# Performance work log

Hardware: AMD Instinct MI355X
Metric: run time of the kernel (lower is better)

The kernel has to match this reference:

```python
import jax, jax.numpy as jnp
import numpy as np

E = 8        # num_workers / experts
D = 1024     # decoder_embed_dim
F = 4096     # decoder_ffn_embed_dim
S, B = 2048, 2
LN_EPS = 1e-5


def setup_inputs() -> dict:
    key = jax.random.key(0)
    ks = jax.random.split(key, 8)
    scale_in = 1.0 / np.sqrt(D)
    scale_ff = 1.0 / np.sqrt(F)
    return {
        "input_features": jax.random.normal(ks[0], (S, B, D), dtype=jnp.float32),
        "centroids": jax.random.normal(ks[1], (E, D), dtype=jnp.float32) * scale_in,  # Linear(D, E, bias=False) weight
        "ln_g": jnp.ones((E, D), dtype=jnp.float32),
        "ln_b": jnp.zeros((E, D), dtype=jnp.float32),
        "W1": jax.random.normal(ks[2], (E, D, F), dtype=jnp.float32) * scale_in,
        "b1": jax.random.normal(ks[3], (E, F), dtype=jnp.float32) * 0.01,
        "W2": jax.random.normal(ks[4], (E, F, D), dtype=jnp.float32) * scale_ff,  # original zero-inits; random for non-trivial reference
        "b2": jax.random.normal(ks[5], (E, D), dtype=jnp.float32) * 0.01,
    }


def _moe_forward(input_features, centroids, ln_g, ln_b, W1, b1, W2, b2):
    s, b, d = input_features.shape
    # [S,B,D] -> transpose(0,1) -> [B,S,D] -> flatten tokens
    x = jnp.swapaxes(input_features, 0, 1).reshape(-1, d)  # [T, D]
    # fp32 gating, top-1 (greedy) assignment; BASE layer does NOT scale by gate prob
    logits = x.astype(jnp.float32) @ centroids.astype(jnp.float32).T  # [T, E]
    assign = jnp.argmax(logits, axis=-1)                              # [T]
    onehot = jax.nn.one_hot(assign, E, dtype=x.dtype)                 # [T, E]
    # dispatch: zero out tokens not assigned to expert e  -> [E, T, D]
    disp = jnp.einsum("te,td->etd", onehot, x)
    # expert-local MoESublayer: xs + ff2(relu(ff1(LN(xs))))
    mu = disp.mean(-1, keepdims=True)
    var = disp.var(-1, keepdims=True)
    xn = (disp - mu) * jax.lax.rsqrt(var + LN_EPS)
    xn = xn * ln_g[:, None, :] + ln_b[:, None, :]
    h = jax.nn.relu(jnp.einsum("etd,edf->etf", xn, W1) + b1[:, None, :])
    y = jnp.einsum("etf,efd->etd", h, W2) + b2[:, None, :]
    y = disp + y  # residual
    # combine: pick assigned expert's output per token (sort+all2all+inverse-sort == identity permutation here)
    out = jnp.einsum("te,etd->td", onehot, y)  # [T, D]
    return jnp.swapaxes(out.reshape(b, s, d), 0, 1)  # back to [S, B, D]


def reference(input_features, centroids, ln_g, ln_b, W1, b1, W2, b2):
    return _moe_forward(input_features, centroids, ln_g, ln_b, W1, b1, W2, b2)
```

## Files before the change

### kernel.cpp

```cpp
#include <hip/hip_runtime.h>
#include <hip/hip_bf16.h>

#define E_ 8
#define D_ 1024
#define F_ 4096
#define S_ 2048
#define B_ 2
#define T_ 4096
#define CAP 1024
#define LN_EPS 1e-5f
#define MAXTAB 40

typedef __attribute__((ext_vector_type(8))) short short8;
typedef __attribute__((ext_vector_type(4))) float f32x4;

__device__ __forceinline__ unsigned short f2bf(float f) {
  __hip_bfloat16 h = __float2bfloat16(f);
  return *reinterpret_cast<unsigned short*>(&h);
}

__global__ __launch_bounds__(256) void gate_ln_kernel(
    const float* __restrict__ x, const float* __restrict__ cent,
    const float* __restrict__ g_, const float* __restrict__ bb_,
    const float* __restrict__ b2_,
    int* __restrict__ counts, int* __restrict__ perm,
    unsigned short* __restrict__ Xb, float* __restrict__ outp) {
  int token = blockIdx.x * 4 + (threadIdx.x >> 6);
  int lane = threadIdx.x & 63;
  int s = token & (S_ - 1), b = token >> 11;
  const float* xr = x + ((size_t)s * B_ + b) * D_;
  float* orow = outp + ((size_t)s * B_ + b) * D_;

  float v[16];
  float acc[E_];
#pragma unroll
  for (int e = 0; e < E_; ++e) acc[e] = 0.f;
  float sum = 0.f, sq = 0.f;
#pragma unroll
  for (int c = 0; c < 4; ++c) {
    f32x4 xv = *(const f32x4*)(xr + c * 256 + lane * 4);
    v[c * 4 + 0] = xv.x; v[c * 4 + 1] = xv.y; v[c * 4 + 2] = xv.z; v[c * 4 + 3] = xv.w;
    sum += xv.x + xv.y + xv.z + xv.w;
    sq += xv.x * xv.x + xv.y * xv.y + xv.z * xv.z + xv.w * xv.w;
#pragma unroll
    for (int e = 0; e < E_; ++e) {
      f32x4 cv = *(const f32x4*)(cent + e * D_ + c * 256 + lane * 4);
      acc[e] += xv.x * cv.x + xv.y * cv.y + xv.z * cv.z + xv.w * cv.w;
    }
  }
#pragma unroll
  for (int off = 32; off > 0; off >>= 1) {
    sum += __shfl_down(sum, off);
    sq += __shfl_down(sq, off);
#pragma unroll
    for (int e = 0; e < E_; ++e) acc[e] += __shfl_down(acc[e], off);
  }
  int best = 0, slot = 0;
  if (lane == 0) {
    float bv = acc[0];
#pragma unroll
    for (int e = 1; e < E_; ++e) if (acc[e] > bv) { bv = acc[e]; best = e; }
    slot = atomicAdd(&counts[best], 1);
    perm[best * CAP + slot] = token;
  }
  best = __shfl(best, 0); slot = __shfl(slot, 0);
  sum = __shfl(sum, 0); sq = __shfl(sq, 0);
  float mu = sum * (1.f / D_);
  float var = sq * (1.f / D_) - mu * mu;
  float rstd = rsqrtf(var + LN_EPS);
  int e = best;
  unsigned short* dst = Xb + (size_t)(e * CAP + slot) * D_;
#pragma unroll
  for (int c = 0; c < 4; ++c) {
    int d = c * 256 + lane * 4;
    f32x4 gv = *(const f32x4*)(g_ + e * D_ + d);
    f32x4 bv = *(const f32x4*)(bb_ + e * D_ + d);
    f32x4 b2v = *(const f32x4*)(b2_ + e * D_ + d);
    ushort4 o;
    o.x = f2bf((v[c * 4 + 0] - mu) * rstd * gv.x + bv.x);
    o.y = f2bf((v[c * 4 + 1] - mu) * rstd * gv.y + bv.y);
    o.z = f2bf((v[c * 4 + 2] - mu) * rstd * gv.z + bv.z);
    o.w = f2bf((v[c * 4 + 3] - mu) * rstd * gv.w + bv.w);
    *(ushort4*)(dst + d) = o;
    f32x4 oi;
    oi.x = v[c * 4 + 0] + b2v.x; oi.y = v[c * 4 + 1] + b2v.y;
    oi.z = v[c * 4 + 2] + b2v.z; oi.w = v[c * 4 + 3] + b2v.w;
    *(f32x4*)(orow + d) = oi;
  }
}

__global__ void prefix_kernel(const int* __restrict__ counts, int* __restrict__ offs,
                              int* __restrict__ tab) {
  if (threadIdx.x == 0) {
    int s = 0, t = 0;
    for (int e = 0; e < E_; ++e) {
      offs[e] = s;
      int nb = (counts[e] + 127) >> 7;
      for (int m = 0; m < nb; ++m) tab[t++] = (e << 16) | m;
      s += counts[e];
    }
    offs[E_] = s;
    for (; t < MAXTAB; ++t) tab[t] = -1;
  }
}

template <int K, int N, int MODE, int KSPLIT>
__global__ __launch_bounds__(256, 3) void moe_gemm_kernel(
    const unsigned short* __restrict__ A,
    const float* __restrict__ W,
    const float* __restrict__ bias,
    const int* __restrict__ counts,
    const int* __restrict__ offs,
    const int* __restrict__ tab,
    const int* __restrict__ perm,
    void* __restrict__ outp) {
  const int tentry = tab[blockIdx.y];
  if (tentry < 0) return;
  const int e = tentry >> 16;
  const int m0 = (tentry & 0xffff) << 7;
  const int cnt = counts[e];
  if (m0 >= cnt) return;
  const int aoff = (MODE == 0) ? e * CAP : offs[e];
  const int hoff = offs[e];
  const int n0 = blockIdx.x * 128;
  const int kstart = blockIdx.z * (K / KSPLIT);
  constexpr int NSTEP = (K / KSPLIT) / 32;
  static_assert(NSTEP >= 4 && (NSTEP % 2) == 0, "NSTEP must be even >= 4");

  const int tid = threadIdx.x;
  const int lane = tid & 63;
  const int wave = tid >> 6;

  __shared__ __align__(16) unsigned short lA[2][4096];
  __shared__ __align__(16) unsigned short lB[2][4096];

  const int ra = tid & 127;
  const int qa = tid >> 7;
  const int arow = aoff + min(m0 + ra, cnt - 1);
  const unsigned short* asrc = A + (size_t)arow * K + kstart + qa * 8;

  const float* wsrc = W + (size_t)e * K * N + (size_t)(kstart + wave * 8) * N + n0 + lane;

  f32x4 acc[4][4] = {};
  const int wr = (wave >> 1) * 64;
  const int wc = (wave & 1) * 64;
  const int fr = lane & 15;
  const int fq = lane >> 4;

  short8 pA00, pA01, pA10, pA11;
  float pBa0[8], pBb0[8], pBa1[8], pBb1[8];

  pA00 = *(const short8*)(asrc);
  pA01 = *(const short8*)(asrc + 16);
#pragma unroll
  for (int j = 0; j < 8; ++j) {
    pBa0[j] = wsrc[(size_t)j * N];
    pBb0[j] = wsrc[(size_t)j * N + 64];
  }
  pA10 = *(const short8*)(asrc + 32);
  pA11 = *(const short8*)(asrc + 48);
  {
    const float* wp_ = wsrc + (size_t)32 * N;
#pragma unroll
    for (int j = 0; j < 8; ++j) {
      pBa1[j] = wp_[(size_t)j * N];
      pBb1[j] = wp_[(size_t)j * N + 64];
    }
  }
  *(short8*)&lA[0][qa * 1024 + ra * 8] = pA00;
  *(short8*)&lA[0][(qa + 2) * 1024 + ra * 8] = pA01;
  {
    short8 c0_, c1_;
#pragma unroll
    for (int j = 0; j < 8; ++j) {
      c0_[j] = (short)f2bf(pBa0[j]);
      c1_[j] = (short)f2bf(pBb0[j]);
    }
    *(short8*)&lB[0][wave * 1024 + lane * 8] = c0_;
    *(short8*)&lB[0][wave * 1024 + (lane + 64) * 8] = c1_;
  }
  asm volatile("s_waitcnt lgkmcnt(0)" ::: "memory");
  __builtin_amdgcn_s_barrier();
  asm volatile("" ::: "memory");

#define STEP_BODY(TV, CUR, NXT)                                                     \
  {                                                                                 \
    const int tv_ = (TV);                                                           \
    if (tv_ + 2 < NSTEP) {            \
      const unsigned short* ap_ = asrc + (tv_ + 2) * 32;                            \
      pA##CUR##0 = *(const short8*)ap_;                                             \
      pA##CUR##1 = *(const short8*)(ap_ + 16);                                      \
      const float* wp_ = wsrc + (size_t)(tv_ + 2) * 32 * N;                         \
      _Pragma("unroll") for (int j = 0; j < 8; ++j) {                               \
        pBa##CUR[j] = wp_[(size_t)j * N];                                           \
        pBb##CUR[j] = wp_[(size_t)j * N + 64];                                      \
      }                                                                             \
    }                                                                               \
    if (tv_ + 1 < NSTEP) {        \
      *(short8*)&lA[NXT][qa * 1024 + ra * 8] = pA##NXT##0;                          \
      *(short8*)&lA[NXT][(qa + 2) * 1024 + ra * 8] = pA##NXT##1;                    \
      short8 c0_, c1_;                                                              \
      _Pragma("unroll") for (int j = 0; j < 8; ++j) {                               \
        c0_[j] = (short)f2bf(pBa##NXT[j]);                                          \
        c1_[j] = (short)f2bf(pBb##NXT[j]);                                          \
      }                                                                             \
      *(short8*)&lB[NXT][wave * 1024 + lane * 8] = c0_;                             \
      *(short8*)&lB[NXT][wave * 1024 + (lane + 64) * 8] = c1_;                      \
    }                                                                               \
    short8 af_[4], bf_[4];                                                          \
    _Pragma("unroll") for (int m = 0; m < 4; ++m)                                   \
        af_[m] = *(const short8*)&lA[CUR][fq * 1024 + (wr + m * 16 + fr) * 8];      \
    _Pragma("unroll") for (int n = 0; n < 4; ++n)                                   \
        bf_[n] = *(const short8*)&lB[CUR][fq * 1024 + (wc + n * 16 + fr) * 8];      \
    __builtin_amdgcn_s_setprio(1);                                                  \
    _Pragma("unroll") for (int m = 0; m < 4; ++m)                                   \
        _Pragma("unroll") for (int n = 0; n < 4; ++n)                               \
            acc[m][n] =                                                             \
                __builtin_amdgcn_mfma_f32_16x16x32_bf16(af_[m], bf_[n],             \
                                                        acc[m][n], 0, 0, 0);        \
    __builtin_amdgcn_s_setprio(0);                                                  \
    asm volatile("s_waitcnt lgkmcnt(0)" ::: "memory");                              \
    __builtin_amdgcn_s_barrier();                                                   \
    asm volatile("" ::: "memory");                                                  \
  }

  for (int t = 0; t < NSTEP; t += 2) {
    STEP_BODY(t, 0, 1);
    STEP_BODY(t + 1, 1, 0);
  }
#undef STEP_BODY

  if (MODE == 0) {
    unsigned short* Hout = (unsigned short*)outp;
    float bv[4];
#pragma unroll
    for (int n = 0; n < 4; ++n) bv[n] = bias[e * N + n0 + wc + n * 16 + fr];
#pragma unroll
    for (int m = 0; m < 4; ++m) {
#pragma unroll
      for (int j = 0; j < 4; ++j) {
        int rg = m0 + wr + m * 16 + fq * 4 + j;
        if (rg < cnt) {
          size_t base = (size_t)(hoff + rg) * N;
#pragma unroll
          for (int n = 0; n < 4; ++n) {
            float hv = acc[m][n][j] + bv[n];
            hv = fmaxf(hv, 0.f);
            Hout[base + n0 + wc + n * 16 + fr] = f2bf(hv);
          }
        }
      }
    }
  } else {
    float* Out = (float*)outp;
#pragma unroll
    for (int m = 0; m < 4; ++m) {
#pragma unroll
      for (int j = 0; j < 4; ++j) {
        int rg = m0 + wr + m * 16 + fq * 4 + j;
        if (rg < cnt) {
          int token = perm[e * CAP + rg];
          size_t base = ((size_t)(token & (S_ - 1)) * B_ + (token >> 11)) * (size_t)D_;
#pragma unroll
          for (int n = 0; n < 4; ++n)
            atomicAdd(&Out[base + n0 + wc + n * 16 + fr], acc[m][n][j]);
        }
      }
    }
  }
}

extern "C" void kernel_launch(void* const* d_in, const int* in_sizes, int n_in,
                              void* d_out, int out_size, void* d_ws, size_t ws_size,
                              hipStream_t stream) {
  const float* x    = (const float*)d_in[0];
  const float* cent = (const float*)d_in[1];
  const float* lng  = (const float*)d_in[2];
  const float* lnb  = (const float*)d_in[3];
  const float* W1   = (const float*)d_in[4];
  const float* b1   = (const float*)d_in[5];
  const float* W2   = (const float*)d_in[6];
  const float* b2   = (const float*)d_in[7];
  float* out = (float*)d_out;

  char* ws = (char*)d_ws;
  int* counts = (int*)(ws + 0);
  int* offs   = (int*)(ws + 64);
  int* tab    = (int*)(ws + 256);
  int* perm   = (int*)(ws + 4096);
  unsigned short* Xb = (unsigned short*)(ws + ((size_t)1 << 18));
  unsigned short* H  = (unsigned short*)(ws + ((size_t)1 << 25));

  if (ws_size < ((size_t)1 << 26)) return;

  hipMemsetAsync(counts, 0, 64, stream);
  gate_ln_kernel<<<T_ / 4, 256, 0, stream>>>(x, cent, lng, lnb, b2, counts, perm, Xb, out);
  prefix_kernel<<<1, 64, 0, stream>>>(counts, offs, tab);
  moe_gemm_kernel<D_, F_, 0, 1><<<dim3(F_ / 128, MAXTAB, 1), 256, 0, stream>>>(
      Xb, W1, b1, counts, offs, tab, perm, (void*)H);
  moe_gemm_kernel<F_, D_, 1, 4><<<dim3(D_ / 128, MAXTAB, 4), 256, 0, stream>>>(
      H, W2, nullptr, counts, offs, tab, perm, (void*)out);
}
```

Before: 279.0 us.

## Flatten MoE GEMM grid into XCD-aware tile table scheduled by prefix kernel

```diff
diff --git a/kernel.cpp b/kernel.cpp
--- a/kernel.cpp
+++ b/kernel.cpp
@@ -9,7 +9,7 @@
 #define T_ 4096
 #define CAP 1024
 #define LN_EPS 1e-5f
-#define MAXTAB 40
+#define NTABF 2048
 
 typedef __attribute__((ext_vector_type(8))) short short8;
 typedef __attribute__((ext_vector_type(4))) float f32x4;
@@ -89,23 +89,55 @@
   }
 }
 
-__global__ void prefix_kernel(const int* __restrict__ counts, int* __restrict__ offs,
-                              int* __restrict__ tab) {
-  if (threadIdx.x == 0) {
-    int s = 0, t = 0;
+__global__ __launch_bounds__(256) void prefix_kernel(
+    const int* __restrict__ counts, int* __restrict__ offs,
+    int* __restrict__ tabF1, int* __restrict__ tabF2) {
+  __shared__ int q[8][256];
+  __shared__ int ql[8];
+  __shared__ int nb[E_];
+  const int tid = threadIdx.x;
+  if (tid == 0) {
+    int s = 0;
     for (int e = 0; e < E_; ++e) {
       offs[e] = s;
-      int nb = (counts[e] + 127) >> 7;
-      for (int m = 0; m < nb; ++m) tab[t++] = (e << 16) | m;
+      nb[e] = (counts[e] + 127) >> 7;
       s += counts[e];
     }
     offs[E_] = s;
-    for (; t < MAXTAB; ++t) tab[t] = -1;
+    for (int x = 0; x < 8; ++x) ql[x] = 0;
+    int g = 0;
+    for (int n = 0; n < F_ / 128; ++n)
+      for (int e = 0; e < E_; ++e) {
+        int x = g & 7; ++g;
+        for (int m = 0; m < nb[e]; ++m) q[x][ql[x]++] = (e << 24) | (m << 16) | (n << 8);
+      }
+  }
+  __syncthreads();
+  for (int i = tid; i < NTABF; i += 256) {
+    int p = i >> 3, x = i & 7;
+    tabF1[i] = (p < ql[x]) ? q[x][p] : -1;
+  }
+  __syncthreads();
+  if (tid == 0) {
+    for (int x = 0; x < 8; ++x) ql[x] = 0;
+    int g = 0;
+    for (int kz = 0; kz < 4; ++kz)
+      for (int n = 0; n < D_ / 128; ++n)
+        for (int e = 0; e < E_; ++e) {
+          int x = g & 7; ++g;
+          for (int m = 0; m < nb[e]; ++m)
+            q[x][ql[x]++] = (e << 24) | (m << 16) | (n << 8) | kz;
+        }
+  }
+  __syncthreads();
+  for (int i = tid; i < NTABF; i += 256) {
+    int p = i >> 3, x = i & 7;
+    tabF2[i] = (p < ql[x]) ? q[x][p] : -1;
   }
 }
 
 template <int K, int N, int MODE, int KSPLIT>
-__global__ __launch_bounds__(256, 3) void moe_gemm_kernel(
+__global__ __launch_bounds__(256, 4) void moe_gemm_kernel(
     const unsigned short* __restrict__ A,
     const float* __restrict__ W,
     const float* __restrict__ bias,
@@ -114,16 +146,16 @@
     const int* __restrict__ tab,
     const int* __restrict__ perm,
     void* __restrict__ outp) {
-  const int tentry = tab[blockIdx.y];
-  if (tentry < 0) return;
-  const int e = tentry >> 16;
-  const int m0 = (tentry & 0xffff) << 7;
+  const int te = tab[blockIdx.x];
+  if (te < 0) return;
+  const int e = te >> 24;
+  const int m0 = ((te >> 16) & 255) << 7;
+  const int n0 = ((te >> 8) & 255) << 7;
+  const int kz = te & 255;
   const int cnt = counts[e];
-  if (m0 >= cnt) return;
   const int aoff = (MODE == 0) ? e * CAP : offs[e];
   const int hoff = offs[e];
-  const int n0 = blockIdx.x * 128;
-  const int kstart = blockIdx.z * (K / KSPLIT);
+  const int kstart = kz * (K / KSPLIT);
   constexpr int NSTEP = (K / KSPLIT) / 32;
   static_assert(NSTEP >= 4 && (NSTEP % 2) == 0, "NSTEP must be even >= 4");
 
@@ -186,7 +218,7 @@
 #define STEP_BODY(TV, CUR, NXT)                                                     \
   {                                                                                 \
     const int tv_ = (TV);                                                           \
-    if (tv_ + 2 < NSTEP) {            \
+    if (tv_ + 2 < NSTEP) {          \
       const unsigned short* ap_ = asrc + (tv_ + 2) * 32;                            \
       pA##CUR##0 = *(const short8*)ap_;                                             \
       pA##CUR##1 = *(const short8*)(ap_ + 16);                                      \
@@ -286,8 +318,9 @@
   char* ws = (char*)d_ws;
   int* counts = (int*)(ws + 0);
   int* offs   = (int*)(ws + 64);
-  int* tab    = (int*)(ws + 256);
-  int* perm   = (int*)(ws + 4096);
+  int* tabF1  = (int*)(ws + 4096);
+  int* tabF2  = (int*)(ws + 12288);
+  int* perm   = (int*)(ws + 20480);
   unsigned short* Xb = (unsigned short*)(ws + ((size_t)1 << 18));
   unsigned short* H  = (unsigned short*)(ws + ((size_t)1 << 25));
 
@@ -295,9 +328,9 @@
 
   hipMemsetAsync(counts, 0, 64, stream);
   gate_ln_kernel<<<T_ / 4, 256, 0, stream>>>(x, cent, lng, lnb, b2, counts, perm, Xb, out);
-  prefix_kernel<<<1, 64, 0, stream>>>(counts, offs, tab);
-  moe_gemm_kernel<D_, F_, 0, 1><<<dim3(F_ / 128, MAXTAB, 1), 256, 0, stream>>>(
-      Xb, W1, b1, counts, offs, tab, perm, (void*)H);
-  moe_gemm_kernel<F_, D_, 1, 4><<<dim3(D_ / 128, MAXTAB, 4), 256, 0, stream>>>(
-      H, W2, nullptr, counts, offs, tab, perm, (void*)out);
-}
+  prefix_kernel<<<1, 256, 0, stream>>>(counts, offs, tabF1, tabF2);
+  moe_gemm_kernel<D_, F_, 0, 1><<<NTABF, 256, 0, stream>>>(
+      Xb, W1, b1, counts, offs, tabF1, perm, (void*)H);
+  moe_gemm_kernel<F_, D_, 1, 4><<<NTABF, 256, 0, stream>>>(
+      H, W2, nullptr, counts, offs, tabF2, perm, (void*)out);
+}
```

Result: slower. 868.7 us (+211.3%).
